# Kernel optimization log

Hardware: AMD Instinct MI355X
Metric: run time of the kernel (lower is better)

The kernel has to match this reference:

```python
import jax, jax.numpy as jnp
import numpy as np

B, N, C, H, D, K = 4, 8192, 384, 12, 2, 256
M = N // K          # 32 members per cluster
CH = C // H         # 32 head dim


def setup_inputs() -> dict:
    key = jax.random.key(0)
    ks = jax.random.split(key, 8)
    pos = jax.random.uniform(ks[0], (B, N, D), jnp.float32) * 100.0
    feat = jax.random.normal(ks[1], (B, N, C), jnp.float32)
    # each batch's points partitioned into K clusters of M members (a permutation)
    perms = jax.vmap(lambda kk: jax.random.permutation(kk, N))(jax.random.split(ks[2], B))
    member_idx = perms.reshape(B * K, M).astype(jnp.int32)               # z x m
    batch_idx = jnp.broadcast_to(
        jnp.repeat(jnp.arange(B, dtype=jnp.int32), K)[:, None], (B * K, M))
    w = 0.02
    qkv_w = jax.random.normal(ks[3], (3 * C, C), jnp.float32) * w
    qkv_b = jnp.zeros((3 * C,), jnp.float32)
    pos_w = jax.random.normal(ks[4], (H, D), jnp.float32) * w
    pos_b = jnp.zeros((H,), jnp.float32)
    proj_w = jax.random.normal(ks[5], (C, C), jnp.float32) * w
    proj_b = jnp.zeros((C,), jnp.float32)
    return dict(pos=pos, feat=feat, member_idx=member_idx, batch_idx=batch_idx,
                qkv_w=qkv_w, qkv_b=qkv_b, pos_w=pos_w, pos_b=pos_b,
                proj_w=proj_w, proj_b=proj_b, k=K)


def reference(pos, feat, member_idx, batch_idx, qkv_w, qkv_b, pos_w, pos_b,
              proj_w, proj_b, k):
    # attend_means=True, mask=None, cluster_score=None, q_subsample_idx=None path
    b, n, c = feat.shape
    d = pos.shape[2]
    h = pos_w.shape[0]
    ch = c // h
    z, m = member_idx.shape
    scale = ch ** -0.5

    qkv = feat @ qkv_w.T + qkv_b            # b,n,3c
    q = qkv[..., :c]                        # b,n,c
    kv = qkv[..., c:]                       # b,n,2c

    pos_orig = pos
    pos_n = pos / jnp.max(pos.reshape(-1, d), axis=0)   # per-coordinate max norm

    # irregular gather of kv / pos per cluster member
    kv_g = kv[batch_idx, member_idx]        # z,m,2c
    pos_g = pos_n[batch_idx, member_idx]    # z,m,d

    # cluster_score=None, mask=None -> uniform weights 1/m (mean over members)
    kv_mean = jnp.mean(kv_g, axis=1).reshape(b, k, 2, h, ch)
    pos_mean = jnp.mean(pos_g, axis=1).reshape(b, k, d)

    key_ = kv_mean[:, :, 0].transpose(0, 2, 1, 3)   # b,h,k,ch
    v = kv_mean[:, :, 1].transpose(0, 2, 1, 3)      # b,h,k,ch
    qh = q.reshape(b, n, h, ch).transpose(0, 2, 1, 3) * scale  # b,h,n,ch

    attn = jnp.einsum('bhnc,bhkc->bhnk', qh, key_)  # b,h,n,k
    rel_pos = pos_mean[:, None, :, :] - pos_orig[:, :, None, :]  # b,n,k,d
    pos_bias = jnp.einsum('bnkd,hd->bhnk', rel_pos, pos_w) + pos_b[None, :, None, None]
    attn = jax.nn.softmax(attn + pos_bias, axis=-1)

    out = jnp.einsum('bhnk,bhkc->bnhc', attn, v).reshape(b, n, c)
    return out @ proj_w.T + proj_b
```

## Files before the change

### kernel.cpp

```cpp
#include <hip/hip_runtime.h>

typedef __attribute__((ext_vector_type(8))) short bf16x8;
typedef __attribute__((ext_vector_type(4))) float f32x4;

#define MFMA16(a,b,c) __builtin_amdgcn_mfma_f32_16x16x32_bf16((a),(b),(c),0,0,0)

__device__ __forceinline__ float b2f(unsigned short u){
  union { unsigned u; float f; } x; x.u = ((unsigned)u) << 16; return x.f;
}
__device__ __forceinline__ unsigned short f2b(float f){
  union { float f; unsigned u; } x; x.f = f;
  unsigned r = x.u + 0x7FFFu + ((x.u >> 16) & 1u);
  return (unsigned short)(r >> 16);
}
__device__ __forceinline__ unsigned pk_rne(float a, float b){
  unsigned ua = __float_as_uint(a), ub = __float_as_uint(b);
  ua += 0x7FFFu + ((ua >> 16) & 1u);
  ub += 0x7FFFu + ((ub >> 16) & 1u);
  return __builtin_amdgcn_perm(ub, ua, 0x07060302u);
}
__device__ __forceinline__ unsigned pk_trunc(float a, float b){
  return __builtin_amdgcn_perm(__float_as_uint(b), __float_as_uint(a), 0x07060302u);
}
__device__ __forceinline__ bf16x8 mk8(unsigned a, unsigned b, unsigned c, unsigned d){
  union { uint4 u; bf16x8 h; } x; x.u = make_uint4(a,b,c,d); return x.h;
}
__device__ __forceinline__ int permp(int cl){
  return (cl & 0xE0) | (((cl >> 2) & 3) << 3) | (((cl >> 4) & 1) << 2) | (cl & 3);
}

typedef __attribute__((address_space(3))) unsigned int lds_u32;
typedef const __attribute__((address_space(1))) unsigned int glb_u32;
__device__ __forceinline__ void gl_lds16(const void* g, void* l){
  __builtin_amdgcn_global_load_lds((glb_u32*)g, (lds_u32*)l, 16, 0, 0);
}

__global__ __launch_bounds__(192) void prep_means_kernel(
    const float* __restrict__ pos, unsigned* __restrict__ pmax,
    const float* __restrict__ qkv_w, unsigned short* __restrict__ qkvwb,
    const float* __restrict__ proj_w, unsigned short* __restrict__ projwb,
    const float* __restrict__ feat,
    const int* __restrict__ member_idx, const int* __restrict__ batch_idx,
    unsigned short* __restrict__ fm, float* __restrict__ pm,
    unsigned short* __restrict__ featb)
{
  int bid = blockIdx.x, t = threadIdx.x;
  if (bid < 1024){
    int g = t / 96, tl = t - g*96;
    int z = bid;
    __shared__ int bases[32];
    __shared__ float4 part[96];
    if (t < 32) bases[t] = batch_idx[z*32 + t]*8192 + member_idx[z*32 + t];
    __syncthreads();
    if (t < 32){
      float2 pp = ((const float2*)pos)[bases[t]];
      #pragma unroll
      for (int off = 16; off >= 1; off >>= 1){
        pp.x += __shfl_xor(pp.x, off, 32);
        pp.y += __shfl_xor(pp.y, off, 32);
      }
      if (t == 0){ pm[z*2] = pp.x*(1.f/32.f); pm[z*2+1] = pp.y*(1.f/32.f); }
    }
    float4 v[16]; int rows[16];
    const float4* f4 = (const float4*)feat;
    #pragma unroll
    for (int m = 0; m < 16; m++){
      rows[m] = bases[g*16 + m];
      v[m] = f4[(long)rows[m]*96 + tl];
    }
    float4 a = {0.f,0.f,0.f,0.f};
    #pragma unroll
    for (int m = 0; m < 16; m++){
      *(uint2*)(featb + (long)rows[m]*384 + tl*4) =
          make_uint2(pk_rne(v[m].x, v[m].y), pk_rne(v[m].z, v[m].w));
      a.x += v[m].x; a.y += v[m].y; a.z += v[m].z; a.w += v[m].w;
    }
    if (g == 1) part[tl] = a;
    __syncthreads();
    if (g == 0){
      float4 b = part[tl];
      a.x += b.x; a.y += b.y; a.z += b.z; a.w += b.w;
      unsigned d0 = pk_rne(a.x*(1.f/32.f), a.y*(1.f/32.f));
      unsigned d1 = pk_rne(a.z*(1.f/32.f), a.w*(1.f/32.f));
      *(uint2*)(fm + (long)z*384 + tl*4) = make_uint2(d0, d1);
    }
  } else if (bid < 1408){
    int u = (bid - 1024)*192 + t;
    const float* in; unsigned short* o; long i;
    if (u < 55296){ in = qkv_w;  o = qkvwb;  i = u; }
    else          { in = proj_w; o = projwb; i = u - 55296; }
    const float4* p = (const float4*)(in + i*8);
    float4 a = p[0], b = p[1];
    *(uint4*)(o + i*8) = make_uint4(pk_rne(a.x,a.y), pk_rne(a.z,a.w),
                                    pk_rne(b.x,b.y), pk_rne(b.z,b.w));
  } else {
    int i = (bid - 1408)*192 + t;
    if (i < 16384){
      float4 v = ((const float4*)pos)[i];
      float m0 = fmaxf(v.x, v.z), m1 = fmaxf(v.y, v.w);
      #pragma unroll
      for (int off = 32; off >= 1; off >>= 1){
        m0 = fmaxf(m0, __shfl_xor(m0, off, 64));
        m1 = fmaxf(m1, __shfl_xor(m1, off, 64));
      }
      if ((t & 63) == 0){
        atomicMax(&pmax[0], __float_as_uint(m0));
        atomicMax(&pmax[1], __float_as_uint(m1));
      }
    }
  }
}

__global__ __launch_bounds__(256) void bias_kernel(
    const float* __restrict__ pm, const float* __restrict__ pmaxf,
    const float* __restrict__ pos_w, const float* __restrict__ pos_b,
    unsigned short* __restrict__ wt)
{
  int idx = blockIdx.x*256 + threadIdx.x;
  int kc = idx & 255;
  int bh = idx >> 8;
  int h = bh % 12;
  float p0 = pm[((bh/12)*256 + kc)*2]   / pmaxf[0];
  float p1 = pm[((bh/12)*256 + kc)*2+1] / pmaxf[1];
  float bias = p0*pos_w[h*2] + p1*pos_w[h*2+1] + pos_b[h];
  wt[(bh << 8) + permp(kc)] = f2b(exp2f(bias * 1.44269504088896340f));
}

__global__ __launch_bounds__(256) void gemm_kv_kernel(
    const unsigned short* __restrict__ A, const unsigned short* __restrict__ W,
    const float* __restrict__ bias, unsigned short* __restrict__ kh,
    unsigned short* __restrict__ vt, const unsigned short* __restrict__ wt)
{
  __shared__ unsigned short As[64*64];
  __shared__ unsigned short Ws[128*64];
  const int N = 768, K = 384;
  int mt = blockIdx.x / 6, nt = blockIdx.x - mt*6;
  int m0 = mt << 6, n0 = nt << 7;
  int tid = threadIdx.x;
  int lane = tid & 63, wave = tid >> 6;
  int wr = (wave >> 1) << 5, wc = (wave & 1) << 6;
  int l15 = lane & 15, quad = lane >> 4;
  int sw = l15 & 7;
  int srow = tid >> 3, sc8 = tid & 7;

  f32x4 acc[2][4];
  #pragma unroll
  for (int i = 0; i < 2; i++)
    #pragma unroll
    for (int j = 0; j < 4; j++) acc[i][j] = (f32x4){0.f,0.f,0.f,0.f};

  for (int k0 = 0; k0 < K; k0 += 64){
    __syncthreads();
    #pragma unroll
    for (int it = 0; it < 2; it++){
      int r = srow + it*32;
      int gc8 = sc8 ^ (r & 7);
      gl_lds16(A + (long)(m0+r)*K + k0 + gc8*8, As + it*2048 + wave*512);
    }
    #pragma unroll
    for (int it = 0; it < 4; it++){
      int r = srow + it*32;
      int gc8 = sc8 ^ (r & 7);
      gl_lds16(W + (long)(n0+r)*K + k0 + gc8*8, Ws + it*2048 + wave*512);
    }
    __syncthreads();
    #pragma unroll
    for (int kk = 0; kk < 2; kk++){
      bf16x8 af[2], bfr[4];
      #pragma unroll
      for (int i = 0; i < 2; i++)
        af[i] = *(const bf16x8*)(As + (wr + i*16 + l15)*64 + (((kk<<2)+quad) ^ sw)*8);
      #pragma unroll
      for (int j = 0; j < 4; j++)
        bfr[j] = *(const bf16x8*)(Ws + (wc + j*16 + l15)*64 + (((kk<<2)+quad) ^ sw)*8);
      #pragma unroll
      for (int i = 0; i < 2; i++)
        #pragma unroll
        for (int j = 0; j < 4; j++)
          acc[i][j] = MFMA16(af[i], bfr[j], acc[i][j]);
    }
  }

  #pragma unroll
  for (int j = 0; j < 4; j++){
    int col = n0 + wc + j*16 + l15;
    float bv = bias[col];
    #pragma unroll
    for (int i = 0; i < 2; i++){
      int row0 = m0 + wr + i*16 + quad*4;
      #pragma unroll
      for (int r = 0; r < 4; r++){
        float v = acc[i][j][r] + bv;
        int row = row0 + r;
        int b = row >> 8, cl = row & 255;
        if (col < 384){
          int h = col >> 5, ch = col & 31;
          kh[((((long)b*12 + h)*256 + cl)*32) + ch] = f2b(v);
        } else {
          int cn = col - 384;
          int h = cn >> 5, ch = cn & 31;
          int pp = permp(cl);
          int c8 = (pp >> 3) ^ (ch & 7);
          float w = b2f(wt[(((long)b*12 + h) << 8) + pp]);
          vt[(((long)b*12 + h)*32 + ch)*256 + c8*8 + (pp & 7)] = f2b(v * w);
        }
      }
    }
  }
}

template<int OUT_F32, int AHM, int CHM>
__global__ __launch_bounds__(512) void gemm_fn_kernel(
    const unsigned short* __restrict__ A, const unsigned short* __restrict__ W,
    const float* __restrict__ bias, void* __restrict__ Cv, float out_scale)
{
  __shared__ unsigned short As[2][64*64];
  __shared__ unsigned short Ws[2][384*64];
  const int K = 384, N = 384;
  int m0 = blockIdx.x << 6;
  int tid = threadIdx.x;
  int lane = tid & 63, wave = tid >> 6;
  int l15 = lane & 15, quad = lane >> 4;
  int sw = l15 & 7;
  int srow = tid >> 3, sc8 = tid & 7;

  f32x4 acc[4][3];
  #pragma unroll
  for (int i = 0; i < 4; i++)
    #pragma unroll
    for (int j = 0; j < 3; j++) acc[i][j] = (f32x4){0.f,0.f,0.f,0.f};

  auto stage = [&](int buf, int k0){
    int gc8 = sc8 ^ (srow & 7);
    const unsigned short* asrc;
    if (AHM){
      int row = m0 + srow;
      int bb = row >> 13, tok = row & 8191;
      int ch = k0 + gc8*8;
      asrc = A + ((((long)(bb*12 + (ch >> 5))) << 13) + tok)*32 + (ch & 31);
    } else {
      asrc = A + (long)(m0+srow)*K + k0 + gc8*8;
    }
    gl_lds16(asrc, &As[buf][wave*512]);
    #pragma unroll
    for (int it = 0; it < 6; it++){
      int r = it*64 + srow;
      int g2 = sc8 ^ (r & 7);
      gl_lds16(W + (long)r*K + k0 + g2*8, &Ws[buf][it*4096 + wave*512]);
    }
  };

  stage(0, 0);
  __syncthreads();
  #pragma unroll
  for (int t = 0; t < 6; t++){
    if (t < 5) stage((t+1)&1, (t+1)*64);
    int cur = t & 1;
    #pragma unroll
    for (int kk = 0; kk < 2; kk++){
      bf16x8 af[4];
      #pragma unroll
      for (int i = 0; i < 4; i++)
        af[i] = *(const bf16x8*)(&As[cur][(i*16 + l15)*64 + (((kk<<2)+quad) ^ sw)*8]);
      #pragma unroll
      for (int j = 0; j < 3; j++){
        bf16x8 bfr = *(const bf16x8*)(&Ws[cur][(wave*48 + j*16 + l15)*64 + (((kk<<2)+quad) ^ sw)*8]);
        #pragma unroll
        for (int i = 0; i < 4; i++)
          acc[i][j] = MFMA16(af[i], bfr, acc[i][j]);
      }
    }
    __syncthreads();
  }

  #pragma unroll
  for (int j = 0; j < 3; j++){
    int col = wave*48 + j*16 + l15;
    float bv = bias[col];
    #pragma unroll
    for (int i = 0; i < 4; i++){
      int row0 = m0 + i*16 + quad*4;
      #pragma unroll
      for (int r = 0; r < 4; r++){
        float v = (acc[i][j][r] + bv) * out_scale;
        int row = row0 + r;
        if (OUT_F32){
          ((float*)Cv)[(long)row*N + col] = v;
        } else if (CHM){
          int bb = row >> 13, tok = row & 8191;
          ((unsigned short*)Cv)[((((long)(bb*12 + (col >> 5))) << 13) + tok)*32 + (col & 31)] = f2b(v);
        } else {
          ((unsigned short*)Cv)[(long)row*N + col] = f2b(v);
        }
      }
    }
  }
}

__global__ __launch_bounds__(256) void attn_kernel(
    const unsigned short* __restrict__ qhm,
    const unsigned short* __restrict__ kh,
    const unsigned short* __restrict__ vt,
    const unsigned short* __restrict__ wt,
    unsigned short* __restrict__ aohm)
{
  __shared__ unsigned short keyS[256*32];
  __shared__ unsigned short vTS[32*256];
  __shared__ unsigned short wS[256];

  int bid = blockIdx.x;
  int chunk = bid & 63;
  int bh = bid >> 6;
  int n0 = chunk << 7;
  int tid = threadIdx.x, lane = tid & 63, wave = tid >> 6;
  int l15 = lane & 15, quad = lane >> 4;
  int sw = l15 & 7;

  const unsigned short* khb = kh + (long)bh*8192;
  const unsigned short* vtb = vt + (long)bh*8192;
  #pragma unroll
  for (int it = 0; it < 4; it++){
    gl_lds16(khb + it*2048 + tid*8, keyS + it*2048 + wave*512);
    gl_lds16(vtb + it*2048 + tid*8, vTS  + it*2048 + wave*512);
  }
  if (tid < 32) *(uint4*)(wS + tid*8) = *(const uint4*)(wt + ((long)bh << 8) + tid*8);

  long qbase = ((long)bh*8192 + n0 + wave*32 + l15)*32 + quad*8;
  bf16x8 aq0 = *(const bf16x8*)(qhm + qbase);
  bf16x8 aq1 = *(const bf16x8*)(qhm + qbase + 512);
  __syncthreads();

  f32x4 o00 = {0.f,0.f,0.f,0.f}, o01 = {0.f,0.f,0.f,0.f}, os0 = {0.f,0.f,0.f,0.f};
  f32x4 o10 = {0.f,0.f,0.f,0.f}, o11 = {0.f,0.f,0.f,0.f}, os1 = {0.f,0.f,0.f,0.f};
  #pragma unroll
  for (int ks = 0; ks < 8; ks++){
    bf16x8 bk0 = *(const bf16x8*)(keyS + ((2*ks  )*16 + l15)*32 + quad*8);
    bf16x8 bk1 = *(const bf16x8*)(keyS + ((2*ks+1)*16 + l15)*32 + quad*8);
    f32x4 z4 = {0.f,0.f,0.f,0.f};
    f32x4 s00 = MFMA16(bk0, aq0, z4);
    f32x4 s01 = MFMA16(bk1, aq0, z4);
    f32x4 s10 = MFMA16(bk0, aq1, z4);
    f32x4 s11 = MFMA16(bk1, aq1, z4);
    #pragma unroll
    for (int c = 0; c < 4; c++){
      s00[c] = exp2f(s00[c]); s01[c] = exp2f(s01[c]);
      s10[c] = exp2f(s10[c]); s11[c] = exp2f(s11[c]);
    }
    bf16x8 pf0 = mk8(pk_trunc(s00[0],s00[1]), pk_trunc(s00[2],s00[3]),
                     pk_trunc(s01[0],s01[1]), pk_trunc(s01[2],s01[3]));
    bf16x8 pf1 = mk8(pk_trunc(s10[0],s10[1]), pk_trunc(s10[2],s10[3]),
                     pk_trunc(s11[0],s11[1]), pk_trunc(s11[2],s11[3]));
    int c8 = (4*ks + quad) ^ sw;
    bf16x8 a0 = *(const bf16x8*)(vTS + l15*256      + c8*8);
    bf16x8 a1 = *(const bf16x8*)(vTS + (16+l15)*256 + c8*8);
    bf16x8 wf = *(const bf16x8*)(wS + ks*32 + quad*8);
    o00 = MFMA16(a0, pf0, o00);
    o01 = MFMA16(a1, pf0, o01);
    os0 = MFMA16(wf, pf0, os0);
    o10 = MFMA16(a0, pf1, o10);
    o11 = MFMA16(a1, pf1, o11);
    os1 = MFMA16(wf, pf1, os1);
  }

  float inv0 = 1.f / os0[0];
  float inv1 = 1.f / os1[0];
  long ob0 = ((long)bh*8192 + n0 + wave*32 + l15)*32 + quad*4;
  *(uint2*)(aohm + ob0)      = make_uint2(pk_rne(o00[0]*inv0, o00[1]*inv0),
                                          pk_rne(o00[2]*inv0, o00[3]*inv0));
  *(uint2*)(aohm + ob0 + 16) = make_uint2(pk_rne(o01[0]*inv0, o01[1]*inv0),
                                          pk_rne(o01[2]*inv0, o01[3]*inv0));
  long ob1 = ob0 + 512;
  *(uint2*)(aohm + ob1)      = make_uint2(pk_rne(o10[0]*inv1, o10[1]*inv1),
                                          pk_rne(o10[2]*inv1, o10[3]*inv1));
  *(uint2*)(aohm + ob1 + 16) = make_uint2(pk_rne(o11[0]*inv1, o11[1]*inv1),
                                          pk_rne(o11[2]*inv1, o11[3]*inv1));
}

extern "C" void kernel_launch(void* const* d_in, const int* in_sizes, int n_in,
                              void* d_out, int out_size, void* d_ws, size_t ws_size,
                              hipStream_t stream)
{
  const float* pos      = (const float*)d_in[0];
  const float* feat     = (const float*)d_in[1];
  const int* member_idx = (const int*)d_in[2];
  const int* batch_idx  = (const int*)d_in[3];
  const float* qkv_w    = (const float*)d_in[4];
  const float* qkv_b    = (const float*)d_in[5];
  const float* pos_w    = (const float*)d_in[6];
  const float* pos_b    = (const float*)d_in[7];
  const float* proj_w   = (const float*)d_in[8];
  const float* proj_b   = (const float*)d_in[9];
  float* out = (float*)d_out;

  char* ws = (char*)d_ws;
  float* pmax           = (float*)ws;
  float* pm             = (float*)(ws + 256);
  unsigned short* fm    = (unsigned short*)(ws + 8704);
  unsigned short* kh    = (unsigned short*)(ws + 795136);
  unsigned short* vt    = (unsigned short*)(ws + 1581568);
  unsigned short* wt    = (unsigned short*)(ws + 2368000);
  unsigned short* q_s   = (unsigned short*)(ws + 2417152);
  unsigned short* ao    = (unsigned short*)(ws + 27582976);
  unsigned short* qkvwb = (unsigned short*)(ws + 52748800);
  unsigned short* projwb= (unsigned short*)(ws + 53633536);
  unsigned short* featb = (unsigned short*)(ws + 53928448);

  hipMemsetAsync(pmax, 0, 8, stream);
  prep_means_kernel<<<1494, 192, 0, stream>>>(pos, (unsigned*)pmax, qkv_w, qkvwb,
                                              proj_w, projwb, feat, member_idx,
                                              batch_idx, fm, pm, featb);
  bias_kernel<<<48, 256, 0, stream>>>(pm, pmax, pos_w, pos_b, wt);
  gemm_kv_kernel<<<96, 256, 0, stream>>>(fm, qkvwb + 384*384, qkv_b + 384, kh, vt, wt);
  gemm_fn_kernel<0,0,1><<<512, 512, 0, stream>>>(featb, qkvwb, qkv_b, q_s,
                                                 0.17677669529663687f * 1.44269504088896340f);
  attn_kernel<<<3072, 256, 0, stream>>>(q_s, kh, vt, wt, ao);
  gemm_fn_kernel<1,1,0><<<512, 512, 0, stream>>>(ao, projwb, proj_b, out, 1.0f);
}
```

Before: 211.4 us.

## Fuse bias, KV GEMM and Q GEMM into one launch; single-buffer GEMMs

Merges the positional-bias kernel, the cluster-mean KV GEMM and the Q projection GEMM into a single kernel of 608 blocks. The first 96 blocks compute the bias weights into shared memory and do the KV GEMM, and the rest do the Q GEMM. This removes two launches and the serial dependency between them. Both the fused Q GEMM and the projection GEMM drop double buffering to single-buffered LDS staging. That shrinks shared memory, but the global-to-LDS load is no longer overlapped with MFMA compute.

After: 192.0 us. 1.1x faster.

```diff
diff --git a/kernel.cpp b/kernel.cpp
--- a/kernel.cpp
+++ b/kernel.cpp
@@ -111,111 +111,163 @@
   }
 }
 
-__global__ __launch_bounds__(256) void bias_kernel(
+__global__ __launch_bounds__(512) void kvq_kernel(
+    const unsigned short* __restrict__ fm,
+    const unsigned short* __restrict__ featb,
+    const unsigned short* __restrict__ qkvwb,
+    const float* __restrict__ qkv_b,
     const float* __restrict__ pm, const float* __restrict__ pmaxf,
     const float* __restrict__ pos_w, const float* __restrict__ pos_b,
-    unsigned short* __restrict__ wt)
-{
-  int idx = blockIdx.x*256 + threadIdx.x;
-  int kc = idx & 255;
-  int bh = idx >> 8;
-  int h = bh % 12;
-  float p0 = pm[((bh/12)*256 + kc)*2]   / pmaxf[0];
-  float p1 = pm[((bh/12)*256 + kc)*2+1] / pmaxf[1];
-  float bias = p0*pos_w[h*2] + p1*pos_w[h*2+1] + pos_b[h];
-  wt[(bh << 8) + permp(kc)] = f2b(exp2f(bias * 1.44269504088896340f));
-}
-
-__global__ __launch_bounds__(256) void gemm_kv_kernel(
-    const unsigned short* __restrict__ A, const unsigned short* __restrict__ W,
-    const float* __restrict__ bias, unsigned short* __restrict__ kh,
-    unsigned short* __restrict__ vt, const unsigned short* __restrict__ wt)
+    unsigned short* __restrict__ kh, unsigned short* __restrict__ vt,
+    unsigned short* __restrict__ wt,
+    unsigned short* __restrict__ q_s, float q_scale)
 {
   __shared__ unsigned short As[64*64];
-  __shared__ unsigned short Ws[128*64];
-  const int N = 768, K = 384;
-  int mt = blockIdx.x / 6, nt = blockIdx.x - mt*6;
-  int m0 = mt << 6, n0 = nt << 7;
+  __shared__ unsigned short Ws[384*64];
+  __shared__ unsigned short wtS[256];
+  const int K = 384;
   int tid = threadIdx.x;
   int lane = tid & 63, wave = tid >> 6;
-  int wr = (wave >> 1) << 5, wc = (wave & 1) << 6;
   int l15 = lane & 15, quad = lane >> 4;
   int sw = l15 & 7;
   int srow = tid >> 3, sc8 = tid & 7;
 
-  f32x4 acc[2][4];
-  #pragma unroll
-  for (int i = 0; i < 2; i++)
-    #pragma unroll
-    for (int j = 0; j < 4; j++) acc[i][j] = (f32x4){0.f,0.f,0.f,0.f};
-
-  for (int k0 = 0; k0 < K; k0 += 64){
-    __syncthreads();
-    #pragma unroll
-    for (int it = 0; it < 2; it++){
-      int r = srow + it*32;
-      int gc8 = sc8 ^ (r & 7);
-      gl_lds16(A + (long)(m0+r)*K + k0 + gc8*8, As + it*2048 + wave*512);
-    }
-    #pragma unroll
-    for (int it = 0; it < 4; it++){
-      int r = srow + it*32;
-      int gc8 = sc8 ^ (r & 7);
-      gl_lds16(W + (long)(n0+r)*K + k0 + gc8*8, Ws + it*2048 + wave*512);
-    }
-    __syncthreads();
-    #pragma unroll
-    for (int kk = 0; kk < 2; kk++){
-      bf16x8 af[2], bfr[4];
-      #pragma unroll
-      for (int i = 0; i < 2; i++)
-        af[i] = *(const bf16x8*)(As + (wr + i*16 + l15)*64 + (((kk<<2)+quad) ^ sw)*8);
-      #pragma unroll
-      for (int j = 0; j < 4; j++)
-        bfr[j] = *(const bf16x8*)(Ws + (wc + j*16 + l15)*64 + (((kk<<2)+quad) ^ sw)*8);
-      #pragma unroll
-      for (int i = 0; i < 2; i++)
-        #pragma unroll
-        for (int j = 0; j < 4; j++)
-          acc[i][j] = MFMA16(af[i], bfr[j], acc[i][j]);
-    }
-  }
-
-  #pragma unroll
-  for (int j = 0; j < 4; j++){
-    int col = n0 + wc + j*16 + l15;
-    float bv = bias[col];
-    #pragma unroll
-    for (int i = 0; i < 2; i++){
-      int row0 = m0 + wr + i*16 + quad*4;
-      #pragma unroll
-      for (int r = 0; r < 4; r++){
-        float v = acc[i][j][r] + bv;
-        int row = row0 + r;
-        int b = row >> 8, cl = row & 255;
-        if (col < 384){
-          int h = col >> 5, ch = col & 31;
-          kh[((((long)b*12 + h)*256 + cl)*32) + ch] = f2b(v);
-        } else {
-          int cn = col - 384;
-          int h = cn >> 5, ch = cn & 31;
-          int pp = permp(cl);
-          int c8 = (pp >> 3) ^ (ch & 7);
-          float w = b2f(wt[(((long)b*12 + h) << 8) + pp]);
-          vt[(((long)b*12 + h)*32 + ch)*256 + c8*8 + (pp & 7)] = f2b(v * w);
+  if (blockIdx.x < 96){
+    int mt = blockIdx.x / 6, nt = blockIdx.x - mt*6;
+    int m0 = mt << 6, n0 = nt << 7;
+    int b = m0 >> 8, cl0 = m0 & 255;
+    const unsigned short* W = qkvwb + 384*384;
+    if (nt >= 3 && tid < 256){
+      int lh = tid >> 6, lc = tid & 63;
+      int h = ((n0 - 384) >> 5) + lh;
+      int cl = cl0 + lc;
+      float p0 = pm[(b*256 + cl)*2]   / pmaxf[0];
+      float p1 = pm[(b*256 + cl)*2+1] / pmaxf[1];
+      float bias = p0*pos_w[h*2] + p1*pos_w[h*2+1] + pos_b[h];
+      unsigned short wv = f2b(exp2f(bias * 1.44269504088896340f));
+      wtS[lh*64 + lc] = wv;
+      wt[(((long)(b*12 + h)) << 8) + permp(cl)] = wv;
+    }
+    int wr = (wave >> 2) << 5, wc = (wave & 3) << 5;
+    f32x4 acc[2][2];
+    #pragma unroll
+    for (int i = 0; i < 2; i++)
+      #pragma unroll
+      for (int j = 0; j < 2; j++) acc[i][j] = (f32x4){0.f,0.f,0.f,0.f};
+
+    for (int k0 = 0; k0 < K; k0 += 64){
+      __syncthreads();
+      int gc8 = sc8 ^ (srow & 7);
+      gl_lds16(fm + (long)(m0+srow)*K + k0 + gc8*8, As + wave*512);
+      #pragma unroll
+      for (int it = 0; it < 2; it++){
+        int r = it*64 + srow;
+        int g2 = sc8 ^ (r & 7);
+        gl_lds16(W + (long)(n0+r)*K + k0 + g2*8, Ws + it*4096 + wave*512);
+      }
+      __syncthreads();
+      #pragma unroll
+      for (int kk = 0; kk < 2; kk++){
+        bf16x8 af[2], bfr[2];
+        #pragma unroll
+        for (int i = 0; i < 2; i++)
+          af[i] = *(const bf16x8*)(As + (wr + i*16 + l15)*64 + (((kk<<2)+quad) ^ sw)*8);
+        #pragma unroll
+        for (int j = 0; j < 2; j++)
+          bfr[j] = *(const bf16x8*)(Ws + (wc + j*16 + l15)*64 + (((kk<<2)+quad) ^ sw)*8);
+        #pragma unroll
+        for (int i = 0; i < 2; i++)
+          #pragma unroll
+          for (int j = 0; j < 2; j++)
+            acc[i][j] = MFMA16(af[i], bfr[j], acc[i][j]);
+      }
+    }
+
+    #pragma unroll
+    for (int j = 0; j < 2; j++){
+      int col = n0 + wc + j*16 + l15;
+      float bv = qkv_b[384 + col];
+      #pragma unroll
+      for (int i = 0; i < 2; i++){
+        #pragma unroll
+        for (int r = 0; r < 4; r++){
+          float v = acc[i][j][r] + bv;
+          int lr = wr + i*16 + quad*4 + r;
+          int cl = cl0 + lr;
+          if (col < 384){
+            int h = col >> 5, ch = col & 31;
+            kh[((((long)b*12 + h)*256 + cl)*32) + ch] = f2b(v);
+          } else {
+            int cn = col - 384;
+            int h = cn >> 5, ch = cn & 31;
+            int pp = permp(cl);
+            int c8 = (pp >> 3) ^ (ch & 7);
+            float w = b2f(wtS[(wave & 3)*64 + lr]);
+            vt[(((long)b*12 + h)*32 + ch)*256 + c8*8 + (pp & 7)] = f2b(v * w);
+          }
         }
       }
     }
-  }
-}
-
-template<int OUT_F32, int AHM, int CHM>
-__global__ __launch_bounds__(512) void gemm_fn_kernel(
+  } else {
+    int m0 = (blockIdx.x - 96) << 6;
+    f32x4 acc[4][3];
+    #pragma unroll
+    for (int i = 0; i < 4; i++)
+      #pragma unroll
+      for (int j = 0; j < 3; j++) acc[i][j] = (f32x4){0.f,0.f,0.f,0.f};
+
+    for (int k0 = 0; k0 < K; k0 += 64){
+      __syncthreads();
+      int gc8 = sc8 ^ (srow & 7);
+      gl_lds16(featb + (long)(m0+srow)*K + k0 + gc8*8, As + wave*512);
+      #pragma unroll
+      for (int it = 0; it < 6; it++){
+        int r = it*64 + srow;
+        int g2 = sc8 ^ (r & 7);
+        gl_lds16(qkvwb + (long)r*K + k0 + g2*8, Ws + it*4096 + wave*512);
+      }
+      __syncthreads();
+      #pragma unroll
+      for (int kk = 0; kk < 2; kk++){
+        bf16x8 af[4];
+        #pragma unroll
+        for (int i = 0; i < 4; i++)
+          af[i] = *(const bf16x8*)(As + (i*16 + l15)*64 + (((kk<<2)+quad) ^ sw)*8);
+        #pragma unroll
+        for (int j = 0; j < 3; j++){
+          bf16x8 bfr = *(const bf16x8*)(Ws + (wave*48 + j*16 + l15)*64 + (((kk<<2)+quad) ^ sw)*8);
+          #pragma unroll
+          for (int i = 0; i < 4; i++)
+            acc[i][j] = MFMA16(af[i], bfr, acc[i][j]);
+        }
+      }
+    }
+
+    #pragma unroll
+    for (int j = 0; j < 3; j++){
+      int col = wave*48 + j*16 + l15;
+      float bv = qkv_b[col];
+      #pragma unroll
+      for (int i = 0; i < 4; i++){
+        int row0 = m0 + i*16 + quad*4;
+        #pragma unroll
+        for (int r = 0; r < 4; r++){
+          float v = (acc[i][j][r] + bv) * q_scale;
+          int row = row0 + r;
+          int bb = row >> 13, tok = row & 8191;
+          q_s[((((long)(bb*12 + (col >> 5))) << 13) + tok)*32 + (col & 31)] = f2b(v);
+        }
+      }
+    }
+  }
+}
+
+__global__ __launch_bounds__(512) void gemm_proj_kernel(
     const unsigned short* __restrict__ A, const unsigned short* __restrict__ W,
-    const float* __restrict__ bias, void* __restrict__ Cv, float out_scale)
+    const float* __restrict__ bias, float* __restrict__ C)
 {
-  __shared__ unsigned short As[2][64*64];
-  __shared__ unsigned short Ws[2][384*64];
+  __shared__ unsigned short As[64*64];
+  __shared__ unsigned short Ws[384*64];
   const int K = 384, N = 384;
   int m0 = blockIdx.x << 6;
   int tid = threadIdx.x;
@@ -230,47 +282,37 @@
     #pragma unroll
     for (int j = 0; j < 3; j++) acc[i][j] = (f32x4){0.f,0.f,0.f,0.f};
 
-  auto stage = [&](int buf, int k0){
-    int gc8 = sc8 ^ (srow & 7);
-    const unsigned short* asrc;
-    if (AHM){
+  for (int k0 = 0; k0 < K; k0 += 64){
+    __syncthreads();
+    {
+      int gc8 = sc8 ^ (srow & 7);
       int row = m0 + srow;
       int bb = row >> 13, tok = row & 8191;
       int ch = k0 + gc8*8;
-      asrc = A + ((((long)(bb*12 + (ch >> 5))) << 13) + tok)*32 + (ch & 31);
-    } else {
-      asrc = A + (long)(m0+srow)*K + k0 + gc8*8;
-    }
-    gl_lds16(asrc, &As[buf][wave*512]);
+      const unsigned short* asrc = A + ((((long)(bb*12 + (ch >> 5))) << 13) + tok)*32 + (ch & 31);
+      gl_lds16(asrc, As + wave*512);
+    }
     #pragma unroll
     for (int it = 0; it < 6; it++){
       int r = it*64 + srow;
       int g2 = sc8 ^ (r & 7);
-      gl_lds16(W + (long)r*K + k0 + g2*8, &Ws[buf][it*4096 + wave*512]);
-    }
-  };
-
-  stage(0, 0);
-  __syncthreads();
-  #pragma unroll
-  for (int t = 0; t < 6; t++){
-    if (t < 5) stage((t+1)&1, (t+1)*64);
-    int cur = t & 1;
+      gl_lds16(W + (long)r*K + k0 + g2*8, Ws + it*4096 + wave*512);
+    }
+    __syncthreads();
     #pragma unroll
     for (int kk = 0; kk < 2; kk++){
       bf16x8 af[4];
       #pragma unroll
       for (int i = 0; i < 4; i++)
-        af[i] = *(const bf16x8*)(&As[cur][(i*16 + l15)*64 + (((kk<<2)+quad) ^ sw)*8]);
+        af[i] = *(const bf16x8*)(As + (i*16 + l15)*64 + (((kk<<2)+quad) ^ sw)*8);
       #pragma unroll
       for (int j = 0; j < 3; j++){
-        bf16x8 bfr = *(const bf16x8*)(&Ws[cur][(wave*48 + j*16 + l15)*64 + (((kk<<2)+quad) ^ sw)*8]);
+        bf16x8 bfr = *(const bf16x8*)(Ws + (wave*48 + j*16 + l15)*64 + (((kk<<2)+quad) ^ sw)*8);
         #pragma unroll
         for (int i = 0; i < 4; i++)
           acc[i][j] = MFMA16(af[i], bfr, acc[i][j]);
       }
     }
-    __syncthreads();
   }
 
   #pragma unroll
@@ -281,18 +323,8 @@
     for (int i = 0; i < 4; i++){
       int row0 = m0 + i*16 + quad*4;
       #pragma unroll
-      for (int r = 0; r < 4; r++){
-        float v = (acc[i][j][r] + bv) * out_scale;
-        int row = row0 + r;
-        if (OUT_F32){
-          ((float*)Cv)[(long)row*N + col] = v;
-        } else if (CHM){
-          int bb = row >> 13, tok = row & 8191;
-          ((unsigned short*)Cv)[((((long)(bb*12 + (col >> 5))) << 13) + tok)*32 + (col & 31)] = f2b(v);
-        } else {
-          ((unsigned short*)Cv)[(long)row*N + col] = f2b(v);
-        }
-      }
+      for (int r = 0; r < 4; r++)
+        C[(long)(row0 + r)*N + col] = acc[i][j][r] + bv;
     }
   }
 }
@@ -409,10 +441,9 @@
   prep_means_kernel<<<1494, 192, 0, stream>>>(pos, (unsigned*)pmax, qkv_w, qkvwb,
                                               proj_w, projwb, feat, member_idx,
                                               batch_idx, fm, pm, featb);
-  bias_kernel<<<48, 256, 0, stream>>>(pm, pmax, pos_w, pos_b, wt);
-  gemm_kv_kernel<<<96, 256, 0, stream>>>(fm, qkvwb + 384*384, qkv_b + 384, kh, vt, wt);
-  gemm_fn_kernel<0,0,1><<<512, 512, 0, stream>>>(featb, qkvwb, qkv_b, q_s,
-                                                 0.17677669529663687f * 1.44269504088896340f);
+  kvq_kernel<<<608, 512, 0, stream>>>(fm, featb, qkvwb, qkv_b, pm, pmax, pos_w, pos_b,
+                                      kh, vt, wt, q_s,
+                                      0.17677669529663687f * 1.44269504088896340f);
   attn_kernel<<<3072, 256, 0, stream>>>(q_s, kh, vt, wt, ao);
-  gemm_fn_kernel<1,1,0><<<512, 512, 0, stream>>>(ao, projwb, proj_b, out, 1.0f);
-}
+  gemm_proj_kernel<<<512, 512, 0, stream>>>(ao, projwb, proj_b, out);
+}
```
